# Optimization experiments

Hardware: AMD Instinct MI355X
Metric: run time of the kernel (lower is better)

Reference implementation:

```python
import jax, jax.numpy as jnp
import numpy as np

D_MODEL = 2048
NUM_HEADS = 16
D_K = D_MODEL // NUM_HEADS
SEQ = 2048
BATCH = 2
THETA = 10000.0


def setup_inputs() -> dict:
    key = jax.random.key(0)
    ks = jax.random.split(key, 5)
    s = 1.0 / np.sqrt(D_MODEL)
    return {
        "x": jax.random.normal(ks[0], (BATCH, SEQ, D_MODEL), jnp.float32),
        "wq": jax.random.normal(ks[1], (D_MODEL, D_MODEL), jnp.float32) * s,
        "wk": jax.random.normal(ks[2], (D_MODEL, D_MODEL), jnp.float32) * s,
        "wv": jax.random.normal(ks[3], (D_MODEL, D_MODEL), jnp.float32) * s,
        "wo": jax.random.normal(ks[4], (D_MODEL, D_MODEL), jnp.float32) * s,
    }


def _rope_tables(seq_len, d_k, theta, dtype):
    pos = jnp.arange(seq_len, dtype=dtype)[:, None]            # [S,1]
    inv = theta ** (-(jnp.arange(0, d_k, 2, dtype=dtype) / d_k))  # [d_k/2]
    ang = pos * inv                                            # [S, d_k/2]
    sin = jnp.repeat(jnp.sin(ang), 2, axis=1)                  # [S, d_k] interleaved
    cos = jnp.repeat(jnp.cos(ang), 2, axis=1)
    return sin, cos


def _apply_rope(x, sin, cos):
    # x: [..., S, d_k]; interleaved-pair rotation
    xp = x.reshape(x.shape[:-1] + (x.shape[-1] // 2, 2))
    swapped = jnp.stack((-xp[..., 1], xp[..., 0]), axis=-1).reshape(x.shape)
    return x * cos + swapped * sin


def reference(x, wq, wk, wv, wo):
    B, S, D = x.shape
    H, dk = NUM_HEADS, D_K
    # projections: weights are (H*dk, D); q/k/v -> [B,H,S,dk]
    q = jnp.einsum("bsd,hkd->bhsk", x, wq.reshape(H, dk, D))
    k = jnp.einsum("bsd,hkd->bhsk", x, wk.reshape(H, dk, D))
    v = jnp.einsum("bsd,hkd->bhsk", x, wv.reshape(H, dk, D))
    sin, cos = _rope_tables(S, dk, THETA, x.dtype)
    q = _apply_rope(q, sin, cos)
    k = _apply_rope(k, sin, cos)
    scores = jnp.einsum("bhqk,bhsk->bhqs", q, k) / jnp.sqrt(jnp.asarray(dk, x.dtype))
    causal = jnp.triu(jnp.ones((S, S), dtype=bool), k=1)
    scores = jnp.where(causal, -jnp.inf, scores)
    attn = jax.nn.softmax(scores, axis=-1)
    out = jnp.einsum("bhqs,bhsv->bqhv", attn, v).reshape(B, S, H * dk)
    return jnp.einsum("bsf,df->bsd", out, wo)
```

## Files before the change

### kernel.cpp

```cpp
#include <hip/hip_runtime.h>
#include <hip/hip_bf16.h>

#define B_  2
#define S_  2048
#define D_  2048
#define H_  16
#define DK_ 128
#define M_  (B_*S_)

typedef unsigned short u16;
typedef short bf16x8 __attribute__((ext_vector_type(8)));
typedef float f32x4  __attribute__((ext_vector_type(4)));

#define NEG_BIG (-1.0e30f)

__device__ __forceinline__ u16 f2bf(float f){
    unsigned int u = __float_as_uint(f);
    unsigned int r = (u + 0x7fffu + ((u >> 16) & 1u)) >> 16;
    return (u16)r;
}

__device__ __forceinline__ uint4 cvt8(const float* p){
    float4 a = *(const float4*)p;
    float4 b = *(const float4*)(p + 4);
    uint4 r;
    r.x = ((unsigned int)f2bf(a.y) << 16) | (unsigned int)f2bf(a.x);
    r.y = ((unsigned int)f2bf(a.w) << 16) | (unsigned int)f2bf(a.z);
    r.z = ((unsigned int)f2bf(b.y) << 16) | (unsigned int)f2bf(b.x);
    r.w = ((unsigned int)f2bf(b.w) << 16) | (unsigned int)f2bf(b.z);
    return r;
}

__device__ __forceinline__ void unpack8(const uint4 v, float* f){
    f[0]=__uint_as_float(v.x<<16); f[1]=__uint_as_float(v.x&0xffff0000u);
    f[2]=__uint_as_float(v.y<<16); f[3]=__uint_as_float(v.y&0xffff0000u);
    f[4]=__uint_as_float(v.z<<16); f[5]=__uint_as_float(v.z&0xffff0000u);
    f[6]=__uint_as_float(v.w<<16); f[7]=__uint_as_float(v.w&0xffff0000u);
}

__device__ __forceinline__ void async16(const void* g, void* l){
    __builtin_amdgcn_global_load_lds(
        (const __attribute__((address_space(1))) void*)g,
        (__attribute__((address_space(3))) void*)l, 16, 0, 0);
}

__global__ __launch_bounds__(256) void cvt_all(
    const float* __restrict__ x,  const float* __restrict__ wq, const float* __restrict__ wk,
    const float* __restrict__ wv, const float* __restrict__ wo,
    u16* __restrict__ xb, u16* __restrict__ wqb, u16* __restrict__ wkb,
    u16* __restrict__ wvb, u16* __restrict__ wob)
{
    int c = blockIdx.x*256 + threadIdx.x;
    const float* src; u16* dst; int lc;
    if      (c < 1048576){ src = x;  dst = xb;  lc = c; }
    else if (c < 1572864){ src = wq; dst = wqb; lc = c - 1048576; }
    else if (c < 2097152){ src = wk; dst = wkb; lc = c - 1572864; }
    else if (c < 2621440){ src = wv; dst = wvb; lc = c - 2097152; }
    else                 { src = wo; dst = wob; lc = c - 2621440; }
    *(uint4*)&dst[(size_t)lc*8] = cvt8(&src[(size_t)lc*8]);
}

template<int MODE>
__global__ __launch_bounds__(256) void gemm_pure(
    const u16* __restrict__ A, const u16* __restrict__ W0, const u16* __restrict__ W1,
    void* __restrict__ C0, void* __restrict__ C1)
{
    __shared__ __align__(16) u16 As[128*32];
    __shared__ __align__(16) u16 Bs[128*32];

    const int tid  = threadIdx.x;
    const int lane = tid & 63;
    const int w    = tid >> 6;
    const int quad = lane >> 4;
    const int l15  = lane & 15;
    const int blockN = blockIdx.x * 128;
    const int blockM = blockIdx.y * 128;

    const u16* Wm; void* Cm;
    if (MODE == 0){ Wm = blockIdx.z ? W1 : W0; Cm = blockIdx.z ? (void*)C1 : (void*)C0; }
    else          { Wm = W0; Cm = C0; }

    const int waveM = (w & 1) * 64;
    const int waveN = (w >> 1) * 64;

    f32x4 acc[16];
    #pragma unroll
    for (int i = 0; i < 16; ++i) acc[i] = (f32x4){0.f,0.f,0.f,0.f};

    for (int k0 = 0; k0 < 2048; k0 += 32){
        __syncthreads();
        #pragma unroll
        for (int it = 0; it < 2; ++it){
            int cc  = tid + it*256;
            int row = cc >> 2;
            int ch  = cc & 3;
            int kb  = k0 + (ch ^ (row & 3))*8;
            const u16* ga;
            if (MODE == 1){
                int g = blockM + row;
                int b = g >> 11, s2 = g & 2047;
                int h = kb >> 7, kk = kb & 127;
                ga = &A[(((size_t)(b*H_ + h))*S_ + s2)*DK_ + kk];
            } else {
                ga = &A[(size_t)(blockM + row)*2048 + kb];
            }
            async16(ga, &As[cc*8]);
            async16(&Wm[(size_t)(blockN + row)*2048 + kb], &Bs[cc*8]);
        }
        __syncthreads();

        bf16x8 af[4], bfv[4];
        #pragma unroll
        for (int mi = 0; mi < 4; ++mi){
            int r = waveM + mi*16 + l15;
            af[mi]  = *(const bf16x8*)&As[r*32 + (quad ^ (r & 3))*8];
        }
        #pragma unroll
        for (int ni = 0; ni < 4; ++ni){
            int r = waveN + ni*16 + l15;
            bfv[ni] = *(const bf16x8*)&Bs[r*32 + (quad ^ (r & 3))*8];
        }
        #pragma unroll
        for (int mi = 0; mi < 4; ++mi)
            #pragma unroll
            for (int ni = 0; ni < 4; ++ni)
                acc[mi*4+ni] = __builtin_amdgcn_mfma_f32_16x16x32_bf16(
                                   af[mi], bfv[ni], acc[mi*4+ni], 0, 0, 0);
    }

    #pragma unroll
    for (int mi = 0; mi < 4; ++mi){
        #pragma unroll
        for (int ni = 0; ni < 4; ++ni){
            #pragma unroll
            for (int r = 0; r < 4; ++r){
                float v = acc[mi*4+ni][r];
                int row = blockM + waveM + mi*16 + quad*4 + r;
                int col = blockN + waveN + ni*16 + l15;
                if (MODE == 0){
                    int b = row >> 11, s2 = row & 2047;
                    int h = col >> 7,  kk = col & 127;
                    ((u16*)Cm)[(((size_t)(b*H_ + h))*S_ + s2)*DK_ + kk] = f2bf(v);
                } else if (MODE == 2){
                    int h = row >> 7,  kk = row & 127;
                    int b = col >> 11, s2 = col & 2047;
                    ((u16*)Cm)[(((size_t)(b*H_ + h))*DK_ + kk)*S_ + s2] = f2bf(v);
                } else {
                    ((float*)Cm)[(size_t)row*2048 + col] = v;
                }
            }
        }
    }
}

template<int MODE>
__global__ __launch_bounds__(256) void gemm_bt(
    const void* __restrict__ Av,
    const float* __restrict__ W0, const float* __restrict__ W1,
    void* __restrict__ C0, void* __restrict__ C1)
{
    __shared__ u16 As[128*40];
    __shared__ u16 Bs[128*40];

    const int tid  = threadIdx.x;
    const int lane = tid & 63;
    const int w    = tid >> 6;
    const int quad = lane >> 4;
    const int l15  = lane & 15;
    const int blockN = blockIdx.x * 128;
    const int blockM = blockIdx.y * 128;

    const float* Wm; void* Cm;
    if (MODE == 0){ Wm = blockIdx.z ? W1 : W0; Cm = blockIdx.z ? (void*)C1 : (void*)C0; }
    else          { Wm = W0; Cm = C0; }

    const int waveM = (w & 1) * 64;
    const int waveN = (w >> 1) * 64;

    f32x4 acc[16];
    #pragma unroll
    for (int i = 0; i < 16; ++i) acc[i] = (f32x4){0.f,0.f,0.f,0.f};

    for (int k0 = 0; k0 < 2048; k0 += 32){
        __syncthreads();
        #pragma unroll
        for (int it = 0; it < 2; ++it){
            int cc  = tid + it*256;
            int row = cc >> 2;
            int ch  = cc & 3;
            int kb  = k0 + ch*8;
            uint4 va;
            if (MODE == 1){
                int g = blockM + row;
                int b = g >> 11, s2 = g & 2047;
                int h = kb >> 7, kk = kb & 127;
                va = *(const uint4*)&((const u16*)Av)[(((size_t)(b*H_ + h))*S_ + s2)*DK_ + kk];
            } else {
                va = cvt8(&((const float*)Av)[(size_t)(blockM+row)*2048 + kb]);
            }
            uint4 vb = cvt8(&Wm[(size_t)(blockN+row)*2048 + kb]);
            *(uint4*)&As[row*40 + ch*8] = va;
            *(uint4*)&Bs[row*40 + ch*8] = vb;
        }
        __syncthreads();

        bf16x8 af[4], bfv[4];
        #pragma unroll
        for (int mi = 0; mi < 4; ++mi)
            af[mi]  = *(const bf16x8*)&As[(waveM + mi*16 + l15)*40 + quad*8];
        #pragma unroll
        for (int ni = 0; ni < 4; ++ni)
            bfv[ni] = *(const bf16x8*)&Bs[(waveN + ni*16 + l15)*40 + quad*8];
        #pragma unroll
        for (int mi = 0; mi < 4; ++mi)
            #pragma unroll
            for (int ni = 0; ni < 4; ++ni)
                acc[mi*4+ni] = __builtin_amdgcn_mfma_f32_16x16x32_bf16(
                                   af[mi], bfv[ni], acc[mi*4+ni], 0, 0, 0);
    }

    #pragma unroll
    for (int mi = 0; mi < 4; ++mi){
        #pragma unroll
        for (int ni = 0; ni < 4; ++ni){
            #pragma unroll
            for (int r = 0; r < 4; ++r){
                float v = acc[mi*4+ni][r];
                int row = blockM + waveM + mi*16 + quad*4 + r;
                int col = blockN + waveN + ni*16 + l15;
                if (MODE == 0){
                    int b = row >> 11, s2 = row & 2047;
                    int h = col >> 7,  kk = col & 127;
                    ((u16*)Cm)[(((size_t)(b*H_ + h))*S_ + s2)*DK_ + kk] = f2bf(v);
                } else if (MODE == 2){
                    int h = row >> 7,  kk = row & 127;
                    int b = col >> 11, s2 = col & 2047;
                    ((u16*)Cm)[(((size_t)(b*H_ + h))*DK_ + kk)*S_ + s2] = f2bf(v);
                } else {
                    ((float*)Cm)[(size_t)row*2048 + col] = v;
                }
            }
        }
    }
}

__global__ __launch_bounds__(256) void rope_kernel(u16* __restrict__ Q, u16* __restrict__ K)
{
    u16* T = blockIdx.y ? K : Q;
    const float osc = blockIdx.y ? 1.0f : 0.12751743f;
    int t  = blockIdx.x * 256 + threadIdx.x;
    int i0 = (t & 15) * 4;
    int s  = (t >> 4) & 2047;
    size_t base = ((size_t)(t >> 4)) * 128 + (size_t)i0 * 2;
    uint4 v = *(const uint4*)&T[base];
    float f[8]; unpack8(v, f);
    const float nl2t = -13.287712379549449f / 64.0f;
    float sf = (float)s;
    unsigned int out[4];
    #pragma unroll
    for (int p = 0; p < 4; ++p){
        float inv = exp2f((float)(i0 + p) * nl2t);
        float ang = sf * inv;
        float sn, cn;
        sincosf(ang, &sn, &cn);
        float e0 = f[2*p], e1 = f[2*p+1];
        float r0 = (e0*cn - e1*sn) * osc;
        float r1 = (e1*cn + e0*sn) * osc;
        out[p] = ((unsigned int)f2bf(r1) << 16) | (unsigned int)f2bf(r0);
    }
    uint4 ov; ov.x = out[0]; ov.y = out[1]; ov.z = out[2]; ov.w = out[3];
    *(uint4*)&T[base] = ov;
}

__global__ __launch_bounds__(512, 4) void attn_mfma(
    const u16* Q, const u16* __restrict__ K,
    const u16* __restrict__ VT, u16* O)
{
    __shared__ __align__(16) u16 Ks[64*128];
    __shared__ __align__(16) u16 Vs[128*64];
    __shared__ __align__(16) u16 Ps[8][16*64];

    const int tid  = threadIdx.x;
    const int bh   = blockIdx.x;
    const int qb   = (int)gridDim.y - 1 - (int)blockIdx.y;
    const int w    = tid >> 6;
    const int lane = tid & 63;
    const int quad = lane >> 4;
    const int l15  = lane & 15;
    const int sw   = l15 & 7;
    const size_t qkb = (size_t)bh * S_ * DK_;

    const int qw = qb*128 + w*16;

    bf16x8 aq[4];
    {
        const u16* qp = &Q[qkb + (size_t)(qw + l15)*128 + quad*8];
        #pragma unroll
        for (int kt = 0; kt < 4; ++kt)
            aq[kt] = *(const bf16x8*)(qp + kt*32);
    }

    f32x4 oa[8];
    #pragma unroll
    for (int vt = 0; vt < 8; ++vt) oa[vt] = (f32x4){0.f,0.f,0.f,0.f};
    float m_i = NEG_BIG, l_i = 0.f;

    const int nkb = 2*qb + 2;
    for (int kb = 0; kb < nkb; ++kb){
        __syncthreads();
        #pragma unroll
        for (int it = 0; it < 2; ++it){
            int cc  = tid + it*512;
            int row = cc >> 4, cl = cc & 15;
            async16(&K[qkb + (size_t)(kb*64 + row)*128 + (size_t)((cl ^ (row & 7))*8)],
                    &Ks[cc*8]);
        }
        #pragma unroll
        for (int it = 0; it < 2; ++it){
            int cc  = tid + it*512;
            int row = cc >> 3, cl = cc & 7;
            async16(&VT[qkb + (size_t)row*S_ + (size_t)(kb*64 + (cl ^ (row & 7))*8)],
                    &Vs[cc*8]);
        }
        __syncthreads();

        if (kb*64 > qw + 15) continue;

        f32x4 s[4];
        __builtin_amdgcn_s_setprio(1);
        #pragma unroll
        for (int nt = 0; nt < 4; ++nt){
            f32x4 a = (f32x4){0.f,0.f,0.f,0.f};
            #pragma unroll
            for (int kt = 0; kt < 4; ++kt){
                bf16x8 ak = *(const bf16x8*)&Ks[(nt*16 + l15)*128 + ((kt*4 + quad) ^ sw)*8];
                a = __builtin_amdgcn_mfma_f32_16x16x32_bf16(ak, aq[kt], a, 0,0,0);
            }
            s[nt] = a;
        }
        __builtin_amdgcn_s_setprio(0);

        if (kb*64 + 63 > qw){
            int qg = qw + l15;
            #pragma unroll
            for (int nt = 0; nt < 4; ++nt)
                #pragma unroll
                for (int rr = 0; rr < 4; ++rr){
                    int jg = kb*64 + nt*16 + quad*4 + rr;
                    if (jg > qg) s[nt][rr] = NEG_BIG;
                }
        }

        float mx = s[0][0];
        #pragma unroll
        for (int nt = 0; nt < 4; ++nt)
            #pragma unroll
            for (int rr = 0; rr < 4; ++rr) mx = fmaxf(mx, s[nt][rr]);
        mx = fmaxf(mx, __shfl_xor(mx, 16, 64));
        mx = fmaxf(mx, __shfl_xor(mx, 32, 64));

        if (!__all((mx - m_i) <= 8.0f)){
            float mn = fmaxf(m_i, mx);
            float al = exp2f(m_i - mn);
            m_i = mn;
            l_i *= al;
            float al4[4];
            #pragma unroll
            for (int rr = 0; rr < 4; ++rr)
                al4[rr] = __shfl(al, (lane & 48) | (quad*4 + rr), 64);
            #pragma unroll
            for (int vt = 0; vt < 8; ++vt)
                #pragma unroll
                for (int rr = 0; rr < 4; ++rr) oa[vt][rr] *= al4[rr];
        }

        float ps = 0.f;
        #pragma unroll
        for (int nt = 0; nt < 4; ++nt)
            #pragma unroll
            for (int rr = 0; rr < 4; ++rr){
                float p = exp2f(s[nt][rr] - m_i);
                s[nt][rr] = p; ps += p;
            }
        ps += __shfl_xor(ps, 16, 64);
        ps += __shfl_xor(ps, 32, 64);
        l_i += ps;

        u16* pw = Ps[w];
        #pragma unroll
        for (int nt = 0; nt < 4; ++nt){
            uint2 pk;
            asm("v_cvt_pk_bf16_f32 %0, %1, %2" : "=v"(pk.x) : "v"(s[nt][0]), "v"(s[nt][1]));
            asm("v_cvt_pk_bf16_f32 %0, %1, %2" : "=v"(pk.y) : "v"(s[nt][2]), "v"(s[nt][3]));
            int c = (nt*2 + (quad >> 1)) ^ sw;
            *(uint2*)&pw[l15*64 + c*8 + (quad & 1)*4] = pk;
        }

        bf16x8 pa[2];
        #pragma unroll
        for (int kt = 0; kt < 2; ++kt)
            pa[kt] = *(const bf16x8*)&pw[l15*64 + ((kt*4 + quad) ^ sw)*8];

        __builtin_amdgcn_s_setprio(1);
        #pragma unroll
        for (int vt = 0; vt < 8; ++vt){
            #pragma unroll
            for (int kt = 0; kt < 2; ++kt){
                bf16x8 bv = *(const bf16x8*)&Vs[(vt*16 + l15)*64 + ((kt*4 + quad) ^ sw)*8];
                oa[vt] = __builtin_amdgcn_mfma_f32_16x16x32_bf16(pa[kt], bv, oa[vt], 0,0,0);
            }
        }
        __builtin_amdgcn_s_setprio(0);
    }

    #pragma unroll
    for (int rr = 0; rr < 4; ++rr){
        float lv = __shfl(l_i, (lane & 48) | (quad*4 + rr), 64);
        float inv = 1.f / lv;
        int qg = qw + quad*4 + rr;
        #pragma unroll
        for (int vt = 0; vt < 8; ++vt)
            O[qkb + (size_t)qg*128 + vt*16 + l15] = f2bf(oa[vt][rr] * inv);
    }
}

extern "C" void kernel_launch(void* const* d_in, const int* in_sizes, int n_in,
                              void* d_out, int out_size, void* d_ws, size_t ws_size,
                              hipStream_t stream)
{
    const float* x  = (const float*)d_in[0];
    const float* wq = (const float*)d_in[1];
    const float* wk = (const float*)d_in[2];
    const float* wv = (const float*)d_in[3];
    const float* wo = (const float*)d_in[4];
    float* out = (float*)d_out;

    const size_t NT = (size_t)B_ * H_ * S_ * DK_;
    const size_t NW = (size_t)D_ * D_;

    if (ws_size >= (size_t)50331648){
        u16* Qw  = (u16*)d_ws;
        u16* Kw  = Qw + NT;
        u16* wvb = Qw + 2*NT;
        u16* wob = wvb + NW;
        u16* xb  = (u16*)d_out;
        u16* wqb = xb + NT;
        u16* wkb = wqb + NW;
        u16* VT  = xb + NT;
        u16* Ow  = Qw;

        cvt_all<<<dim3(12288), 256, 0, stream>>>(x, wq, wk, wv, wo,
                                                 xb, wqb, wkb, wvb, wob);
        gemm_pure<0><<<dim3(16, 32, 2), 256, 0, stream>>>(xb, wqb, wkb, Qw, Kw);
        gemm_pure<2><<<dim3(32, 16, 1), 256, 0, stream>>>(wvb, xb, nullptr, VT, nullptr);
        rope_kernel<<<dim3(4096, 2), 256, 0, stream>>>(Qw, Kw);
        attn_mfma<<<dim3(32, 16), 512, 0, stream>>>(Qw, Kw, VT, Ow);
        gemm_pure<1><<<dim3(16, 32, 1), 256, 0, stream>>>(Ow, wob, nullptr, out, nullptr);
    } else {
        u16* Qw  = (u16*)d_ws;
        u16* Vtd = (u16*)d_out;
        u16* Kw  = (u16*)d_out + NT;
        u16* Ow  = Qw;
        gemm_bt<0><<<dim3(16, 32, 2), 256, 0, stream>>>(x, wq, wk, Qw, Kw);
        gemm_bt<2><<<dim3(32, 16, 1), 256, 0, stream>>>(wv, x, nullptr, Vtd, nullptr);
        rope_kernel<<<dim3(4096, 2), 256, 0, stream>>>(Qw, Kw);
        attn_mfma<<<dim3(32, 16), 512, 0, stream>>>(Qw, Kw, Vtd, Ow);
        gemm_bt<1><<<dim3(16, 32, 1), 256, 0, stream>>>(Ow, wo, nullptr, out, nullptr);
    }
}
```

Baseline: 416.6 us.

## Replace 128x128 bf16 GEMM with 256x256 tile, 4-stage async LDS ring

Replaces the projection GEMM with a 512-thread kernel computing 256x256 output tiles. It uses a 4-deep LDS ring of async global-to-LDS copies with explicit vmcnt waits, one barrier per k-step, a new XOR swizzle, and s_setprio around the MFMA blocks. The goal is to hide global load latency and raise data reuse per tile. In exchange, each thread holds twice as many accumulators and the kernel needs 128KB of LDS, so occupancy is lower and fewer blocks fill the GPU.

```diff
diff --git a/kernel.cpp b/kernel.cpp
--- a/kernel.cpp
+++ b/kernel.cpp
@@ -61,12 +61,140 @@
 }
 
 template<int MODE>
-__global__ __launch_bounds__(256) void gemm_pure(
+__global__ __launch_bounds__(512, 2) void gemm256(
     const u16* __restrict__ A, const u16* __restrict__ W0, const u16* __restrict__ W1,
     void* __restrict__ C0, void* __restrict__ C1)
 {
-    __shared__ __align__(16) u16 As[128*32];
-    __shared__ __align__(16) u16 Bs[128*32];
+    __shared__ __align__(16) u16 ring[4][2][8192];
+
+    const int tid  = threadIdx.x;
+    const int lane = tid & 63;
+    const int w    = tid >> 6;
+    const int quad = lane >> 4;
+    const int l15  = lane & 15;
+    const int wM   = w & 1;
+    const int wN   = w >> 1;
+    const int blockN = blockIdx.x * 256;
+    const int blockM = blockIdx.y * 256;
+
+    const u16* Wm; void* Cm;
+    if (MODE == 0){ Wm = blockIdx.z ? W1 : W0; Cm = blockIdx.z ? (void*)C1 : (void*)C0; }
+    else          { Wm = W0; Cm = C0; }
+
+    const int cswz = quad ^ ((l15 >> 1) & 3);
+
+    f32x4 acc[32];
+    #pragma unroll
+    for (int i = 0; i < 32; ++i) acc[i] = (f32x4){0.f,0.f,0.f,0.f};
+
+    auto stage = [&](int t){
+        const int k0 = t * 32;
+        u16* la = (u16*)&ring[t & 3][0][0];
+        u16* lb = (u16*)&ring[t & 3][1][0];
+        #pragma unroll
+        for (int it = 0; it < 2; ++it){
+            int cc  = it*512 + tid;
+            int row = cc >> 2;
+            int g   = (cc & 3) ^ ((cc >> 3) & 3);
+            int kb  = k0 + g*8;
+            const u16* ga;
+            if (MODE == 1){
+                int rg = blockM + row;
+                int b = rg >> 11, s2 = rg & 2047;
+                int h = kb >> 7,  kk = kb & 127;
+                ga = &A[(((size_t)(b*H_ + h))*S_ + s2)*DK_ + kk];
+            } else {
+                ga = &A[(size_t)(blockM + row)*2048 + kb];
+            }
+            async16(ga, la + cc*8);
+            async16(&Wm[(size_t)(blockN + row)*2048 + kb], lb + cc*8);
+        }
+    };
+
+    stage(0); stage(1); stage(2);
+    asm volatile("s_waitcnt vmcnt(8)" ::: "memory");
+    __builtin_amdgcn_s_barrier();
+    __builtin_amdgcn_sched_barrier(0);
+
+    for (int t = 0; t < 64; ++t){
+        const u16* la = (const u16*)&ring[t & 3][0][0];
+        const u16* lb = (const u16*)&ring[t & 3][1][0];
+
+        if (t <= 60) stage(t + 3);
+
+        bf16x8 bfv[4], af[4];
+        #pragma unroll
+        for (int ni = 0; ni < 4; ++ni)
+            bfv[ni] = *(const bf16x8*)&lb[(wN*64 + ni*16 + l15)*32 + cswz*8];
+        #pragma unroll
+        for (int mi = 0; mi < 4; ++mi)
+            af[mi]  = *(const bf16x8*)&la[(wM*128 + mi*16 + l15)*32 + cswz*8];
+
+        __builtin_amdgcn_s_setprio(1);
+        #pragma unroll
+        for (int mi = 0; mi < 4; ++mi)
+            #pragma unroll
+            for (int ni = 0; ni < 4; ++ni)
+                acc[mi*4+ni] = __builtin_amdgcn_mfma_f32_16x16x32_bf16(
+                                   af[mi], bfv[ni], acc[mi*4+ni], 0, 0, 0);
+        __builtin_amdgcn_s_setprio(0);
+
+        #pragma unroll
+        for (int mi = 0; mi < 4; ++mi)
+            af[mi]  = *(const bf16x8*)&la[(wM*128 + 64 + mi*16 + l15)*32 + cswz*8];
+
+        __builtin_amdgcn_s_setprio(1);
+        #pragma unroll
+        for (int mi = 0; mi < 4; ++mi)
+            #pragma unroll
+            for (int ni = 0; ni < 4; ++ni)
+                acc[16 + mi*4+ni] = __builtin_amdgcn_mfma_f32_16x16x32_bf16(
+                                   af[mi], bfv[ni], acc[16 + mi*4+ni], 0, 0, 0);
+        __builtin_amdgcn_s_setprio(0);
+
+        if (t <= 60)      { asm volatile("s_waitcnt vmcnt(8)" ::: "memory"); }
+        else if (t == 61) { asm volatile("s_waitcnt vmcnt(4)" ::: "memory"); }
+        else if (t == 62) { asm volatile("s_waitcnt vmcnt(0)" ::: "memory"); }
+        __builtin_amdgcn_s_barrier();
+        __builtin_amdgcn_sched_barrier(0);
+    }
+
+    #pragma unroll
+    for (int hf = 0; hf < 2; ++hf){
+        #pragma unroll
+        for (int mi = 0; mi < 4; ++mi){
+            #pragma unroll
+            for (int ni = 0; ni < 4; ++ni){
+                #pragma unroll
+                for (int r = 0; r < 4; ++r){
+                    float v = acc[hf*16 + mi*4+ni][r];
+                    int row = blockM + wM*128 + hf*64 + mi*16 + quad*4 + r;
+                    int col = blockN + wN*64 + ni*16 + l15;
+                    if (MODE == 0){
+                        int b = row >> 11, s2 = row & 2047;
+                        int h = col >> 7,  kk = col & 127;
+                        ((u16*)Cm)[(((size_t)(b*H_ + h))*S_ + s2)*DK_ + kk] = f2bf(v);
+                    } else if (MODE == 2){
+                        int h = row >> 7,  kk = row & 127;
+                        int b = col >> 11, s2 = col & 2047;
+                        ((u16*)Cm)[(((size_t)(b*H_ + h))*DK_ + kk)*S_ + s2] = f2bf(v);
+                    } else {
+                        ((float*)Cm)[(size_t)row*2048 + col] = v;
+                    }
+                }
+            }
+        }
+    }
+}
+
+template<int MODE>
+__global__ __launch_bounds__(256) void gemm_bt(
+    const void* __restrict__ Av,
+    const float* __restrict__ W0, const float* __restrict__ W1,
+    void* __restrict__ C0, void* __restrict__ C1)
+{
+    __shared__ u16 As[128*40];
+    __shared__ u16 Bs[128*40];
 
     const int tid  = threadIdx.x;
     const int lane = tid & 63;
@@ -76,7 +204,7 @@
     const int blockN = blockIdx.x * 128;
     const int blockM = blockIdx.y * 128;
 
-    const u16* Wm; void* Cm;
+    const float* Wm; void* Cm;
     if (MODE == 0){ Wm = blockIdx.z ? W1 : W0; Cm = blockIdx.z ? (void*)C1 : (void*)C0; }
     else          { Wm = W0; Cm = C0; }
 
@@ -94,32 +222,29 @@
             int cc  = tid + it*256;
             int row = cc >> 2;
             int ch  = cc & 3;
-            int kb  = k0 + (ch ^ (row & 3))*8;
-            const u16* ga;
+            int kb  = k0 + ch*8;
+            uint4 va;
             if (MODE == 1){
                 int g = blockM + row;
                 int b = g >> 11, s2 = g & 2047;
                 int h = kb >> 7, kk = kb & 127;
-                ga = &A[(((size_t)(b*H_ + h))*S_ + s2)*DK_ + kk];
+                va = *(const uint4*)&((const u16*)Av)[(((size_t)(b*H_ + h))*S_ + s2)*DK_ + kk];
             } else {
-                ga = &A[(size_t)(blockM + row)*2048 + kb];
-            }
-            async16(ga, &As[cc*8]);
-            async16(&Wm[(size_t)(blockN + row)*2048 + kb], &Bs[cc*8]);
+                va = cvt8(&((const float*)Av)[(size_t)(blockM+row)*2048 + kb]);
+            }
+            uint4 vb = cvt8(&Wm[(size_t)(blockN+row)*2048 + kb]);
+            *(uint4*)&As[row*40 + ch*8] = va;
+            *(uint4*)&Bs[row*40 + ch*8] = vb;
         }
         __syncthreads();
 
         bf16x8 af[4], bfv[4];
         #pragma unroll
-        for (int mi = 0; mi < 4; ++mi){
-            int r = waveM + mi*16 + l15;
-            af[mi]  = *(const bf16x8*)&As[r*32 + (quad ^ (r & 3))*8];
-        }
-        #pragma unroll
-        for (int ni = 0; ni < 4; ++ni){
-            int r = waveN + ni*16 + l15;
-            bfv[ni] = *(const bf16x8*)&Bs[r*32 + (quad ^ (r & 3))*8];
-        }
+        for (int mi = 0; mi < 4; ++mi)
+            af[mi]  = *(const bf16x8*)&As[(waveM + mi*16 + l15)*40 + quad*8];
+        #pragma unroll
+        for (int ni = 0; ni < 4; ++ni)
+            bfv[ni] = *(const bf16x8*)&Bs[(waveN + ni*16 + l15)*40 + quad*8];
         #pragma unroll
         for (int mi = 0; mi < 4; ++mi)
             #pragma unroll
@@ -153,97 +278,6 @@
     }
 }
 
-template<int MODE>
-__global__ __launch_bounds__(256) void gemm_bt(
-    const void* __restrict__ Av,
-    const float* __restrict__ W0, const float* __restrict__ W1,
-    void* __restrict__ C0, void* __restrict__ C1)
-{
-    __shared__ u16 As[128*40];
-    __shared__ u16 Bs[128*40];
-
-    const int tid  = threadIdx.x;
-    const int lane = tid & 63;
-    const int w    = tid >> 6;
-    const int quad = lane >> 4;
-    const int l15  = lane & 15;
-    const int blockN = blockIdx.x * 128;
-    const int blockM = blockIdx.y * 128;
-
-    const float* Wm; void* Cm;
-    if (MODE == 0){ Wm = blockIdx.z ? W1 : W0; Cm = blockIdx.z ? (void*)C1 : (void*)C0; }
-    else          { Wm = W0; Cm = C0; }
-
-    const int waveM = (w & 1) * 64;
-    const int waveN = (w >> 1) * 64;
-
-    f32x4 acc[16];
-    #pragma unroll
-    for (int i = 0; i < 16; ++i) acc[i] = (f32x4){0.f,0.f,0.f,0.f};
-
-    for (int k0 = 0; k0 < 2048; k0 += 32){
-        __syncthreads();
-        #pragma unroll
-        for (int it = 0; it < 2; ++it){
-            int cc  = tid + it*256;
-            int row = cc >> 2;
-            int ch  = cc & 3;
-            int kb  = k0 + ch*8;
-            uint4 va;
-            if (MODE == 1){
-                int g = blockM + row;
-                int b = g >> 11, s2 = g & 2047;
-                int h = kb >> 7, kk = kb & 127;
-                va = *(const uint4*)&((const u16*)Av)[(((size_t)(b*H_ + h))*S_ + s2)*DK_ + kk];
-            } else {
-                va = cvt8(&((const float*)Av)[(size_t)(blockM+row)*2048 + kb]);
-            }
-            uint4 vb = cvt8(&Wm[(size_t)(blockN+row)*2048 + kb]);
-            *(uint4*)&As[row*40 + ch*8] = va;
-            *(uint4*)&Bs[row*40 + ch*8] = vb;
-        }
-        __syncthreads();
-
-        bf16x8 af[4], bfv[4];
-        #pragma unroll
-        for (int mi = 0; mi < 4; ++mi)
-            af[mi]  = *(const bf16x8*)&As[(waveM + mi*16 + l15)*40 + quad*8];
-        #pragma unroll
-        for (int ni = 0; ni < 4; ++ni)
-            bfv[ni] = *(const bf16x8*)&Bs[(waveN + ni*16 + l15)*40 + quad*8];
-        #pragma unroll
-        for (int mi = 0; mi < 4; ++mi)
-            #pragma unroll
-            for (int ni = 0; ni < 4; ++ni)
-                acc[mi*4+ni] = __builtin_amdgcn_mfma_f32_16x16x32_bf16(
-                                   af[mi], bfv[ni], acc[mi*4+ni], 0, 0, 0);
-    }
-
-    #pragma unroll
-    for (int mi = 0; mi < 4; ++mi){
-        #pragma unroll
-        for (int ni = 0; ni < 4; ++ni){
-            #pragma unroll
-            for (int r = 0; r < 4; ++r){
-                float v = acc[mi*4+ni][r];
-                int row = blockM + waveM + mi*16 + quad*4 + r;
-                int col = blockN + waveN + ni*16 + l15;
-                if (MODE == 0){
-                    int b = row >> 11, s2 = row & 2047;
-                    int h = col >> 7,  kk = col & 127;
-                    ((u16*)Cm)[(((size_t)(b*H_ + h))*S_ + s2)*DK_ + kk] = f2bf(v);
-                } else if (MODE == 2){
-                    int h = row >> 7,  kk = row & 127;
-                    int b = col >> 11, s2 = col & 2047;
-                    ((u16*)Cm)[(((size_t)(b*H_ + h))*DK_ + kk)*S_ + s2] = f2bf(v);
-                } else {
-                    ((float*)Cm)[(size_t)row*2048 + col] = v;
-                }
-            }
-        }
-    }
-}
-
 __global__ __launch_bounds__(256) void rope_kernel(u16* __restrict__ Q, u16* __restrict__ K)
 {
     u16* T = blockIdx.y ? K : Q;
@@ -451,11 +485,11 @@
 
         cvt_all<<<dim3(12288), 256, 0, stream>>>(x, wq, wk, wv, wo,
                                                  xb, wqb, wkb, wvb, wob);
-        gemm_pure<0><<<dim3(16, 32, 2), 256, 0, stream>>>(xb, wqb, wkb, Qw, Kw);
-        gemm_pure<2><<<dim3(32, 16, 1), 256, 0, stream>>>(wvb, xb, nullptr, VT, nullptr);
+        gemm256<0><<<dim3(8, 16, 2), 512, 0, stream>>>(xb, wqb, wkb, Qw, Kw);
+        gemm256<2><<<dim3(16, 8, 1), 512, 0, stream>>>(wvb, xb, nullptr, VT, nullptr);
         rope_kernel<<<dim3(4096, 2), 256, 0, stream>>>(Qw, Kw);
         attn_mfma<<<dim3(32, 16), 512, 0, stream>>>(Qw, Kw, VT, Ow);
-        gemm_pure<1><<<dim3(16, 32, 1), 256, 0, stream>>>(Ow, wob, nullptr, out, nullptr);
+        gemm256<1><<<dim3(8, 16, 1), 512, 0, stream>>>(Ow, wob, nullptr, out, nullptr);
     } else {
         u16* Qw  = (u16*)d_ws;
         u16* Vtd = (u16*)d_out;
```

After: 399.3 us. -4.1%, faster.
